# Optimization experiments

Hardware: AMD Instinct MI355X
Metric: run time of the kernel (lower is better)

## Reference

```python
import jax, jax.numpy as jnp
import numpy as np

BLANK = 0
DELAY_SCALE = 1.0
TEMPERATURE = 1.0
NEG = -1e30  # finite stand-in for -inf (safe under autodiff of cumlogsumexp)


def _delay_cost_zero(B, Tm, U1, act_lens):
    # delay_values[b, t, u] = t / act_len[b], constant over u  (delay_func='zero')
    dv = jnp.arange(Tm, dtype=jnp.float32)[None, :] / act_lens.astype(jnp.float32)[:, None]
    return jnp.broadcast_to(dv[:, :, None], (B, Tm, U1))


def _rnnt_delay_loss(acts, labels, act_lens, label_lens):
    # RNN-T forward-backward DP over the (T,U) lattice + expected-delay cost,
    # matching warp_rnnt.gpu_rnnt_delay. acts: (B,T,U+1,V) logits.
    B, Tm, U1, V = acts.shape
    U = U1 - 1
    lp = jax.nn.log_softmax(acts / TEMPERATURE, axis=-1)
    blank_lp = lp[..., BLANK]                                   # (B,Tm,U1)
    lab = jnp.broadcast_to(labels.astype(jnp.int32)[:, None, :, None], (B, Tm, U, 1))
    label_lp = jnp.take_along_axis(lp[:, :, :U, :], lab, axis=3)[..., 0]  # (B,Tm,U)
    # exclusive cumsum of label log-probs along u: Lc[...,u] = sum_{j<u} label_lp[...,j]
    Lc = jnp.concatenate([jnp.zeros((B, Tm, 1), lp.dtype), jnp.cumsum(label_lp, axis=2)], axis=2)

    # ---- alpha: alpha[t,u] = LSE(alpha[t-1,u]+blank[t-1,u], alpha[t,u-1]+label[t,u-1])
    # within-row recursion solved in closed form: alpha[t] = Lc[t] + cumlogsumexp(x - Lc[t])
    # where x[u] = alpha[t-1,u] + blank[t-1,u].
    x0 = jnp.where(jnp.arange(U1)[None, :] == 0, 0.0, NEG).astype(lp.dtype)
    alpha0 = Lc[:, 0] + jax.lax.cumlogsumexp(jnp.broadcast_to(x0, (B, U1)) - Lc[:, 0], axis=1)

    def fstep(a_prev, xs):
        bl, lc = xs
        a = lc + jax.lax.cumlogsumexp(a_prev + bl - lc, axis=1)
        return a, a

    xs = (jnp.swapaxes(blank_lp[:, :-1], 0, 1), jnp.swapaxes(Lc[:, 1:], 0, 1))
    _, alphas = jax.lax.scan(fstep, alpha0, xs)
    alpha = jnp.concatenate([alpha0[None], alphas], axis=0).swapaxes(0, 1)  # (B,Tm,U1)

    bi = jnp.arange(B)
    t_last = act_lens - 1
    logZ = alpha[bi, t_last, label_lens] + blank_lp[bi, t_last, label_lens]  # (B,)

    # ---- beta: beta[t,u] = LSE(blank[t,u]+beta[t+1,u], label[t,u]+beta[t,u+1], exit[t,u])
    # exit only at the per-example corner (act_len-1, label_len) with final blank.
    t_idx = jnp.arange(Tm)[None, :, None]
    u_idx = jnp.arange(U1)[None, None, :]
    exit_lp = jnp.where((t_idx == t_last[:, None, None]) & (u_idx == label_lens[:, None, None]), blank_lp, NEG)

    def bstep(b_next, xs):
        bl, ex, lc = xs
        y = jnp.logaddexp(bl + b_next, ex)
        b = -lc + jax.lax.cumlogsumexp(y + lc, axis=1, reverse=True)
        return b, b

    xsb = (jnp.swapaxes(blank_lp, 0, 1), jnp.swapaxes(exit_lp, 0, 1), jnp.swapaxes(Lc, 0, 1))
    _, betas = jax.lax.scan(bstep, jnp.full((B, U1), NEG, lp.dtype), xsb, reverse=True)
    beta = betas.swapaxes(0, 1)  # (B,Tm,U1)

    # ---- expected delay: posterior of emit transition (t,u)->(t,u+1)
    delay_values = _delay_cost_zero(B, Tm, U1, act_lens)
    gamma = jnp.exp(alpha[:, :, :U] + label_lp + beta[:, :, 1:] - logZ[:, None, None])  # (B,Tm,U)
    loss_delay = jnp.sum(gamma * delay_values[:, :, :U], axis=(1, 2))
    loss_rnnt = -logZ
    loss_total = loss_rnnt + DELAY_SCALE * loss_delay
    # reduction='sum'
    return loss_total.sum(), loss_rnnt.sum(), loss_delay.sum()


def setup_inputs() -> dict:
    key = jax.random.key(0)
    k1, k2, k3, k4 = jax.random.split(key, 4)
    B, Tm, U, V = 16, 256, 64, 512
    acts = jax.random.normal(k1, (B, Tm, U + 1, V), dtype=jnp.float32)
    labels = jax.random.randint(k2, (B, U), 1, V, dtype=jnp.int32)  # non-blank targets
    act_lens = jax.random.randint(k3, (B,), Tm // 2, Tm + 1, dtype=jnp.int32)
    label_lens = jax.random.randint(k4, (B,), U // 2, U + 1, dtype=jnp.int32)
    return {"acts": acts, "labels": labels, "act_lens": act_lens, "label_lens": label_lens}


def reference(acts, labels, act_lens, label_lens):
    return _rnnt_delay_loss(acts, labels, act_lens, label_lens)
```

## Files before the change

kernel.cpp:

```cpp
#include <hip/hip_runtime.h>
#include <hip/hip_bf16.h>

#define BB   16
#define TM   256
#define UU   64
#define U1   65
#define VV   512
#define ND   320
#define WROW 128
#define NEGF (-1e30f)
#define LOG2E 1.4426950408889634f
#define LN2   0.6931471805599453f

#if __has_builtin(__builtin_amdgcn_exp2f)
__device__ __forceinline__ float aexp2(float x) { return __builtin_amdgcn_exp2f(x); }
#else
__device__ __forceinline__ float aexp2(float x) { return exp2f(x); }
#endif
#if __has_builtin(__builtin_amdgcn_logf)
__device__ __forceinline__ float alog2(float x) { return __builtin_amdgcn_logf(x); }
#else
__device__ __forceinline__ float alog2(float x) { return log2f(x); }
#endif

__device__ __forceinline__ float lae2(float x, float y) {
    float m = fmaxf(x, y);
    return m + alog2(1.0f + aexp2(-fabsf(x - y)));
}
__device__ __forceinline__ float readlane_f(float v, int l) {
    return __int_as_float(__builtin_amdgcn_readlane(__float_as_int(v), l));
}
__device__ __forceinline__ float shfl_up1(float v) {
    return __int_as_float(__builtin_amdgcn_update_dpp(
        __float_as_int(v), __float_as_int(v), 0x138, 0xF, 0xF, false));
}
__device__ __forceinline__ float shfl_dn1(float v) {
    return __int_as_float(__builtin_amdgcn_update_dpp(
        __float_as_int(v), __float_as_int(v), 0x130, 0xF, 0xF, false));
}
__device__ __forceinline__ void st_clamped(float* __restrict__ s, int t, int lane, float v) {
    int tc = t < -1 ? -1 : t;
    tc = tc > 256 ? 256 : tc;
    s[(tc + 1) * UU + lane] = v;
}

__global__ void k_fill(float* __restrict__ p, int n4) {
    int i = blockIdx.x * blockDim.x + threadIdx.x;
    if (i < n4) reinterpret_cast<float4*>(p)[i] = make_float4(NEGF, NEGF, NEGF, NEGF);
}

__global__ __launch_bounds__(256) void k_lse(const float* __restrict__ acts,
                                             const int* __restrict__ labels,
                                             float* __restrict__ Aarr,
                                             float* __restrict__ Barr,
                                             float* __restrict__ p6arr,
                                             float* __restrict__ bl64) {
    int wid = (blockIdx.x << 2) + (threadIdx.x >> 6);
    if (wid >= BB * TM * U1) return;
    int lane = threadIdx.x & 63;
    const float* base = acts + (size_t)wid * VV;
    float4 va = *reinterpret_cast<const float4*>(base + lane * 4);
    float4 vb = *reinterpret_cast<const float4*>(base + 256 + lane * 4);
    float m = fmaxf(fmaxf(fmaxf(va.x, va.y), fmaxf(va.z, va.w)),
                    fmaxf(fmaxf(vb.x, vb.y), fmaxf(vb.z, vb.w)));
#pragma unroll
    for (int o = 32; o; o >>= 1) m = fmaxf(m, __shfl_xor(m, o));
    float s = __expf(va.x - m) + __expf(va.y - m) + __expf(va.z - m) + __expf(va.w - m)
            + __expf(vb.x - m) + __expf(vb.y - m) + __expf(vb.z - m) + __expf(vb.w - m);
#pragma unroll
    for (int o = 32; o; o >>= 1) s += __shfl_xor(s, o);
    float lse = m + __logf(s);
    if (lane == 0) {
        int u  = wid % U1;
        int bt = wid / U1;
        int t  = bt % TM;
        int b  = bt / TM;
        float blank = (va.x - lse) * LOG2E;
        if (u < UU) {
            int r = t + u;
            int li = labels[b * UU + u];
            float lab = (base[li] - lse) * LOG2E;
            size_t row = ((size_t)b * ND + r) * WROW;
            *reinterpret_cast<float2*>(Barr + row + 2 * u) = make_float2(lab, blank);
            Aarr[row + 2 * u] = blank;
            if (u < 63) Aarr[row + 2 * u + 3] = lab;
            else        p6arr[b * ND + r]     = lab;
        } else {
            bl64[b * TM + t] = blank;
        }
    }
}

__device__ __forceinline__ void load8s(float2 (&B)[8], const float* base,
                                       int row0, int step, int lane) {
#pragma unroll
    for (int j = 0; j < 8; ++j)
        B[j] = *reinterpret_cast<const float2*>(base + (size_t)(row0 + j * step) * WROW + 2 * lane);
}

template<bool N64>
__device__ __forceinline__ void alpha_chunk(const float2 (&B)[8], int ss0,
    int lane, int ssCap64,
    const float* __restrict__ s_bl64p, const float* __restrict__ s_p6,
    float* __restrict__ s_alpha,
    float& a, float& a64, float& cap64)
{
    float c64r[8], p6r[8], aout[8];
    if (N64) {
#pragma unroll
        for (int j = 0; j < 8; ++j) {
            int i64 = ss0 + j - 64; i64 = i64 < 0 ? 0 : i64;
            c64r[j] = s_bl64p[i64];
            p6r[j]  = s_p6[ss0 + j - 1];
        }
    }
#pragma unroll
    for (int j = 0; j < 8; ++j) {
        const float left = shfl_up1(a);
        const float anew = lae2(a + B[j].x, left + B[j].y);
        if (N64) {
            const float a63u = readlane_f(a, 63);
            a64 = lae2(a64 + c64r[j], a63u + p6r[j]);
            if (ss0 + j == ssCap64) cap64 = a64;
        }
        a = anew;
        aout[j] = anew;
    }
#pragma unroll
    for (int j = 0; j < 8; ++j)
        st_clamped(s_alpha, ss0 + j - lane, lane, aout[j]);
}

template<bool N64>
__device__ __forceinline__ void beta_chunk(const float2 (&B)[8], int ss0,
    int lane, int ssExit, int ssExit64, int L,
    const float* __restrict__ s_bl64p, float* __restrict__ s_pr,
    float& bt, float& b64)
{
    float c64r[8], bout[8];
    if (N64) {
#pragma unroll
        for (int j = 0; j < 8; ++j) {
            int i64 = ss0 - j - 63; i64 = i64 < 0 ? 0 : i64;
            c64r[j] = s_bl64p[i64];
        }
    }
#pragma unroll
    for (int j = 0; j < 8; ++j) {
        const int ss = ss0 - j;
        float right = shfl_dn1(bt);
        right = (lane == 63) ? (N64 ? b64 : NEGF) : right;
        const float pr = B[j].x + right;
        float bnew = lae2(B[j].y + bt, pr);
        if (ss == ssExit) {
            if (lane == L) bnew = lae2(bnew, B[j].y);
        }
        if (N64) {
            float b64n = b64 + c64r[j];
            if (ss == ssExit64) b64n = lae2(b64n, c64r[j]);
            b64 = b64n;
        }
        bt = bnew; bout[j] = pr;
    }
#pragma unroll
    for (int j = 0; j < 8; ++j)
        st_clamped(s_pr, ss0 - j - lane, lane, bout[j]);
}

template<bool N64>
__device__ __forceinline__ float alpha_sweep(const float* __restrict__ Aarr,
    int lane, int t_last, int L,
    const float* __restrict__ s_bl64p, const float* __restrict__ s_p6,
    float* __restrict__ s_alpha)
{
    float a = (lane == 0) ? 0.0f : NEGF;
    float a64 = NEGF, cap64 = NEGF;
    const int ssCap64 = t_last + 64;
    float2 R0[8], R1[8], R2[8], R3[8], R4[8];
    load8s(R0, Aarr, 0, 1, lane);  load8s(R1, Aarr, 8, 1, lane);
    load8s(R2, Aarr, 16, 1, lane); load8s(R3, Aarr, 24, 1, lane);
    load8s(R4, Aarr, 32, 1, lane);
    for (int c = 0; c < 40; c += 5) {
        alpha_chunk<N64>(R0, c * 8 + 1, lane, ssCap64, s_bl64p, s_p6, s_alpha, a, a64, cap64);
        if (c + 5 < 40) load8s(R0, Aarr, (c + 5) * 8, 1, lane);
        alpha_chunk<N64>(R1, (c + 1) * 8 + 1, lane, ssCap64, s_bl64p, s_p6, s_alpha, a, a64, cap64);
        if (c + 6 < 40) load8s(R1, Aarr, (c + 6) * 8, 1, lane);
        alpha_chunk<N64>(R2, (c + 2) * 8 + 1, lane, ssCap64, s_bl64p, s_p6, s_alpha, a, a64, cap64);
        if (c + 7 < 40) load8s(R2, Aarr, (c + 7) * 8, 1, lane);
        alpha_chunk<N64>(R3, (c + 3) * 8 + 1, lane, ssCap64, s_bl64p, s_p6, s_alpha, a, a64, cap64);
        if (c + 8 < 40) load8s(R3, Aarr, (c + 8) * 8, 1, lane);
        alpha_chunk<N64>(R4, (c + 4) * 8 + 1, lane, ssCap64, s_bl64p, s_p6, s_alpha, a, a64, cap64);
        if (c + 9 < 40) load8s(R4, Aarr, (c + 9) * 8, 1, lane);
    }
    return cap64;
}

template<bool N64>
__device__ __forceinline__ void beta_sweep(const float* __restrict__ Barr,
    int lane, int ssExit, int ssExit64, int L,
    const float* __restrict__ s_bl64p, float* __restrict__ s_pr)
{
    float bt = NEGF, b64 = NEGF;
    float2 R0[8], R1[8], R2[8], R3[8], R4[8];
    load8s(R0, Barr, 319, -1, lane); load8s(R1, Barr, 311, -1, lane);
    load8s(R2, Barr, 303, -1, lane); load8s(R3, Barr, 295, -1, lane);
    load8s(R4, Barr, 287, -1, lane);
    for (int c = 0; c < 40; c += 5) {
        beta_chunk<N64>(R0, 319 - c * 8, lane, ssExit, ssExit64, L, s_bl64p, s_pr, bt, b64);
        if (c + 5 < 40) load8s(R0, Barr, 319 - (c + 5) * 8, -1, lane);
        beta_chunk<N64>(R1, 319 - (c + 1) * 8, lane, ssExit, ssExit64, L, s_bl64p, s_pr, bt, b64);
        if (c + 6 < 40) load8s(R1, Barr, 319 - (c + 6) * 8, -1, lane);
        beta_chunk<N64>(R2, 319 - (c + 2) * 8, lane, ssExit, ssExit64, L, s_bl64p, s_pr, bt, b64);
        if (c + 7 < 40) load8s(R2, Barr, 319 - (c + 7) * 8, -1, lane);
        beta_chunk<N64>(R3, 319 - (c + 3) * 8, lane, ssExit, ssExit64, L, s_bl64p, s_pr, bt, b64);
        if (c + 8 < 40) load8s(R3, Barr, 319 - (c + 8) * 8, -1, lane);
        beta_chunk<N64>(R4, 319 - (c + 4) * 8, lane, ssExit, ssExit64, L, s_bl64p, s_pr, bt, b64);
        if (c + 9 < 40) load8s(R4, Barr, 319 - (c + 9) * 8, -1, lane);
    }
}

__global__ __launch_bounds__(128, 1) void k_dp(const float* __restrict__ Aarr_,
                                               const float* __restrict__ Barr_,
                                               const float* __restrict__ p6arr_,
                                               const float* __restrict__ bl64_,
                                               const int* __restrict__ act_lens,
                                               const int* __restrict__ label_lens,
                                               float* __restrict__ partials) {
    __shared__ float s_alpha[258 * UU];
    __shared__ float s_pr[258 * UU];
    __shared__ float s_bl64p[TM + 2];
    __shared__ float s_p6[ND];
    __shared__ float s_logZ;
    __shared__ float s_red[2];
    const int b    = blockIdx.x;
    const int tid  = threadIdx.x;
    const int lane = tid & 63;
    const int wv   = tid >> 6;
    const float* Aarr = Aarr_ + (size_t)b * ND * WROW;
    const float* Barr = Barr_ + (size_t)b * ND * WROW;

    if (tid == 0) { s_bl64p[0] = NEGF; s_bl64p[TM + 1] = NEGF; }
    for (int i = tid; i < TM; i += 128) s_bl64p[i + 1] = bl64_[b * TM + i];
    for (int i = tid; i < ND; i += 128) s_p6[i] = p6arr_[b * ND + i];
    __syncthreads();

    const int T = act_lens[b];
    const int L = label_lens[b];
    const int t_last = T - 1;

    if (wv == 0) {
        if (lane == 0) s_alpha[1 * UU + 0] = 0.0f;
        float aE;
        if (L == UU) {
            aE = alpha_sweep<true >(Aarr, lane, t_last, L, s_bl64p, s_p6, s_alpha);
        } else {
            alpha_sweep<false>(Aarr, lane, t_last, L, s_bl64p, s_p6, s_alpha);
            aE = s_alpha[(t_last + 1) * UU + L];
        }
        const float blankLast = (L < UU) ? Aarr[(size_t)(t_last + L) * WROW + 2 * L]
                                         : s_bl64p[t_last + 1];
        if (lane == 0) s_logZ = aE + blankLast;
    } else {
        const int ssExit   = t_last + L;
        const int ssExit64 = (L == UU) ? (t_last + 64) : -1;
        if (L == UU) beta_sweep<true >(Barr, lane, ssExit, ssExit64, L, s_bl64p, s_pr);
        else         beta_sweep<false>(Barr, lane, ssExit, ssExit64, L, s_bl64p, s_pr);
    }
    __syncthreads();

    const float logZ = s_logZ;
    const float invT = 1.0f / (float)T;
    float dsum = 0.0f;
#pragma unroll 8
    for (int idx = tid; idx < TM * UU; idx += 128) {
        const int t = idx >> 6;
        dsum = __fmaf_rn(aexp2(s_alpha[idx + UU] + s_pr[idx + UU] - logZ),
                         (float)t * invT, dsum);
    }
#pragma unroll
    for (int o = 32; o; o >>= 1) dsum += __shfl_xor(dsum, o);
    if (lane == 0) s_red[wv] = dsum;
    __syncthreads();
    if (tid == 0) {
        partials[2 * b + 0] = -logZ * LN2;
        partials[2 * b + 1] = s_red[0] + s_red[1];
    }
}

__global__ void k_reduce(const float* __restrict__ partials, float* __restrict__ out) {
    if (threadIdx.x == 0 && blockIdx.x == 0) {
        float rn = 0.0f, dl = 0.0f;
        for (int b = 0; b < BB; ++b) {
            rn += partials[2 * b + 0];
            dl += partials[2 * b + 1];
        }
        out[0] = rn + dl;
        out[1] = rn;
        out[2] = dl;
    }
}

extern "C" void kernel_launch(void* const* d_in, const int* in_sizes, int n_in,
                              void* d_out, int out_size, void* d_ws, size_t ws_size,
                              hipStream_t stream) {
    const float* acts       = (const float*)d_in[0];
    const int*   labels     = (const int*)d_in[1];
    const int*   act_lens   = (const int*)d_in[2];
    const int*   label_lens = (const int*)d_in[3];

    float* ws       = (float*)d_ws;
    float* Aarr     = ws;
    float* Barr     = Aarr + (size_t)BB * ND * WROW;
    float* p6arr    = Barr + (size_t)BB * ND * WROW;
    float* bl64     = p6arr + BB * ND;
    float* partials = bl64 + BB * TM;

    const int nfill4 = (2 * BB * ND * WROW + BB * ND) / 4;
    k_fill<<<(nfill4 + 255) / 256, 256, 0, stream>>>(ws, nfill4);

    const int rows = BB * TM * U1;
    k_lse<<<(rows + 3) / 4, 256, 0, stream>>>(acts, labels, Aarr, Barr, p6arr, bl64);
    k_dp<<<BB, 128, 0, stream>>>(Aarr, Barr, p6arr, bl64, act_lens, label_lens, partials);
    k_reduce<<<1, 64, 0, stream>>>(partials, (float*)d_out);
}
```

Measured before the change: 140.8 us.

## Run RNN-T DP in scaled probability space instead of log space

The alpha/beta recursions now work on probabilities with per-wave exponent rescaling every four steps, instead of log-add-exp. Each step becomes an FMA plus a DPP shuffle rather than an exp and a log, and k_lse stores probabilities instead of log-probs. The separate column-64 tracking is replaced by a precomputed cumulative log-blank boundary for beta, and logZ is read from beta at the origin. This adds scale bookkeeping (a DPP max-reduction and a readlane) on the serial chain, and it risks precision loss or underflow compared with log-space arithmetic.

```diff
diff --git a/kernel.cpp b/kernel.cpp
--- a/kernel.cpp
+++ b/kernel.cpp
@@ -9,8 +9,7 @@
 #define ND   320
 #define WROW 128
 #define NEGF (-1e30f)
-#define LOG2E 1.4426950408889634f
-#define LN2   0.6931471805599453f
+#define LN2  0.6931471805599453f
 
 #if __has_builtin(__builtin_amdgcn_exp2f)
 __device__ __forceinline__ float aexp2(float x) { return __builtin_amdgcn_exp2f(x); }
@@ -22,11 +21,8 @@
 #else
 __device__ __forceinline__ float alog2(float x) { return log2f(x); }
 #endif
-
-__device__ __forceinline__ float lae2(float x, float y) {
-    float m = fmaxf(x, y);
-    return m + alog2(1.0f + aexp2(-fabsf(x - y)));
-}
+__device__ __forceinline__ float alog2c(float x) { return fmaxf(alog2(x), NEGF); }
+
 __device__ __forceinline__ float readlane_f(float v, int l) {
     return __int_as_float(__builtin_amdgcn_readlane(__float_as_int(v), l));
 }
@@ -37,6 +33,29 @@
 __device__ __forceinline__ float shfl_dn1(float v) {
     return __int_as_float(__builtin_amdgcn_update_dpp(
         __float_as_int(v), __float_as_int(v), 0x130, 0xF, 0xF, false));
+}
+template<int CTRL>
+__device__ __forceinline__ float dppmax(float v) {
+    int x = __builtin_amdgcn_update_dpp(__float_as_int(v), __float_as_int(v),
+                                        CTRL, 0xF, 0xF, false);
+    return fmaxf(v, __int_as_float(x));
+}
+__device__ __forceinline__ void applyscale(float& v, int& E, float cmx) {
+    float m = cmx;
+    m = dppmax<0x111>(m);
+    m = dppmax<0x112>(m);
+    m = dppmax<0x114>(m);
+    m = dppmax<0x118>(m);
+    m = dppmax<0x142>(m);
+    m = dppmax<0x143>(m);
+    int smx = __builtin_amdgcn_readlane(__float_as_int(m), 63);
+    if (smx != 0) {
+        int e = ((smx >> 23) & 0xFF) - 127;
+        if (e < -27) e = -27;
+        float sc = __int_as_float((227 - e) << 23);
+        v *= sc;
+        E += e - 100;
+    }
 }
 __device__ __forceinline__ void st_clamped(float* __restrict__ s, int t, int lane, float v) {
     int tc = t < -1 ? -1 : t;
@@ -44,16 +63,10 @@
     s[(tc + 1) * UU + lane] = v;
 }
 
-__global__ void k_fill(float* __restrict__ p, int n4) {
-    int i = blockIdx.x * blockDim.x + threadIdx.x;
-    if (i < n4) reinterpret_cast<float4*>(p)[i] = make_float4(NEGF, NEGF, NEGF, NEGF);
-}
-
 __global__ __launch_bounds__(256) void k_lse(const float* __restrict__ acts,
                                              const int* __restrict__ labels,
                                              float* __restrict__ Aarr,
                                              float* __restrict__ Barr,
-                                             float* __restrict__ p6arr,
                                              float* __restrict__ bl64) {
     int wid = (blockIdx.x << 2) + (threadIdx.x >> 6);
     if (wid >= BB * TM * U1) return;
@@ -69,24 +82,23 @@
             + __expf(vb.x - m) + __expf(vb.y - m) + __expf(vb.z - m) + __expf(vb.w - m);
 #pragma unroll
     for (int o = 32; o; o >>= 1) s += __shfl_xor(s, o);
-    float lse = m + __logf(s);
+    float rcp_s = 1.0f / s;
     if (lane == 0) {
         int u  = wid % U1;
         int bt = wid / U1;
         int t  = bt % TM;
         int b  = bt / TM;
-        float blank = (va.x - lse) * LOG2E;
+        float pblank = __expf(va.x - m) * rcp_s;
         if (u < UU) {
             int r = t + u;
             int li = labels[b * UU + u];
-            float lab = (base[li] - lse) * LOG2E;
+            float plab = __expf(base[li] - m) * rcp_s;
             size_t row = ((size_t)b * ND + r) * WROW;
-            *reinterpret_cast<float2*>(Barr + row + 2 * u) = make_float2(lab, blank);
-            Aarr[row + 2 * u] = blank;
-            if (u < 63) Aarr[row + 2 * u + 3] = lab;
-            else        p6arr[b * ND + r]     = lab;
+            *reinterpret_cast<float2*>(Barr + row + 2 * u) = make_float2(plab, pblank);
+            Aarr[row + 2 * u] = pblank;
+            if (u < 63) Aarr[row + 2 * u + 3] = plab;
         } else {
-            bl64[b * TM + t] = blank;
+            bl64[b * TM + t] = pblank;
         }
     }
 }
@@ -98,138 +110,94 @@
         B[j] = *reinterpret_cast<const float2*>(base + (size_t)(row0 + j * step) * WROW + 2 * lane);
 }
 
-template<bool N64>
-__device__ __forceinline__ void alpha_chunk(const float2 (&B)[8], int ss0,
-    int lane, int ssCap64,
-    const float* __restrict__ s_bl64p, const float* __restrict__ s_p6,
-    float* __restrict__ s_alpha,
-    float& a, float& a64, float& cap64)
+__device__ __forceinline__ void alpha_chunk(const float2 (&B)[8], int ss0, int ck,
+    int lane, float* __restrict__ s_alpha, float* __restrict__ s_Ea,
+    float& a, int& E)
 {
-    float c64r[8], p6r[8], aout[8];
-    if (N64) {
-#pragma unroll
-        for (int j = 0; j < 8; ++j) {
-            int i64 = ss0 + j - 64; i64 = i64 < 0 ? 0 : i64;
-            c64r[j] = s_bl64p[i64];
-            p6r[j]  = s_p6[ss0 + j - 1];
-        }
-    }
-#pragma unroll
-    for (int j = 0; j < 8; ++j) {
+    float aout[8];
+    float cmx = a;
+    if (lane == 0) s_Ea[2 * ck] = (float)E;
+#pragma unroll
+    for (int j = 0; j < 4; ++j) {
         const float left = shfl_up1(a);
-        const float anew = lae2(a + B[j].x, left + B[j].y);
-        if (N64) {
-            const float a63u = readlane_f(a, 63);
-            a64 = lae2(a64 + c64r[j], a63u + p6r[j]);
-            if (ss0 + j == ssCap64) cap64 = a64;
-        }
-        a = anew;
-        aout[j] = anew;
-    }
+        a = __fmaf_rn(a, B[j].x, left * B[j].y);
+        aout[j] = a;
+    }
+    applyscale(a, E, cmx);
+    cmx = a;
+    if (lane == 0) s_Ea[2 * ck + 1] = (float)E;
+#pragma unroll
+    for (int j = 4; j < 8; ++j) {
+        const float left = shfl_up1(a);
+        a = __fmaf_rn(a, B[j].x, left * B[j].y);
+        aout[j] = a;
+    }
+    applyscale(a, E, cmx);
 #pragma unroll
     for (int j = 0; j < 8; ++j)
         st_clamped(s_alpha, ss0 + j - lane, lane, aout[j]);
 }
 
 template<bool N64>
-__device__ __forceinline__ void beta_chunk(const float2 (&B)[8], int ss0,
-    int lane, int ssExit, int ssExit64, int L,
-    const float* __restrict__ s_bl64p, float* __restrict__ s_pr,
-    float& bt, float& b64)
+__device__ __forceinline__ void beta_chunk(const float2 (&B)[8], int ss0, int ck,
+    int lane, int ssExit, int L,
+    float* __restrict__ s_pr, float* __restrict__ s_Eb,
+    const float* __restrict__ s_b64, float& b, int& E)
 {
-    float c64r[8], bout[8];
+    float prout[8];
+    float cmx = b;
+    if (lane == 0) s_Eb[2 * ck] = (float)E;
+    float r64[8];
     if (N64) {
 #pragma unroll
-        for (int j = 0; j < 8; ++j) {
-            int i64 = ss0 - j - 63; i64 = i64 < 0 ? 0 : i64;
-            c64r[j] = s_bl64p[i64];
-        }
-    }
-#pragma unroll
-    for (int j = 0; j < 8; ++j) {
+        for (int j = 0; j < 4; ++j)
+            r64[j] = aexp2(fminf(s_b64[ss0 - j + 1] - (float)E, 126.0f));
+    }
+#pragma unroll
+    for (int j = 0; j < 4; ++j) {
         const int ss = ss0 - j;
-        float right = shfl_dn1(bt);
-        right = (lane == 63) ? (N64 ? b64 : NEGF) : right;
-        const float pr = B[j].x + right;
-        float bnew = lae2(B[j].y + bt, pr);
-        if (ss == ssExit) {
-            if (lane == L) bnew = lae2(bnew, B[j].y);
-        }
-        if (N64) {
-            float b64n = b64 + c64r[j];
-            if (ss == ssExit64) b64n = lae2(b64n, c64r[j]);
-            b64 = b64n;
-        }
-        bt = bnew; bout[j] = pr;
-    }
+        float right = shfl_dn1(b);
+        right = (lane == 63) ? (N64 ? r64[j] : 0.0f) : right;
+        const float pr = B[j].x * right;
+        b = __fmaf_rn(b, B[j].y, pr);
+        if (ss == ssExit) { if (lane == L) b += B[j].y; }
+        prout[j] = pr;
+    }
+    applyscale(b, E, cmx);
+    cmx = b;
+    if (lane == 0) s_Eb[2 * ck + 1] = (float)E;
+    if (N64) {
+#pragma unroll
+        for (int j = 4; j < 8; ++j)
+            r64[j] = aexp2(fminf(s_b64[ss0 - j + 1] - (float)E, 126.0f));
+    }
+#pragma unroll
+    for (int j = 4; j < 8; ++j) {
+        const int ss = ss0 - j;
+        float right = shfl_dn1(b);
+        right = (lane == 63) ? (N64 ? r64[j] : 0.0f) : right;
+        const float pr = B[j].x * right;
+        b = __fmaf_rn(b, B[j].y, pr);
+        if (ss == ssExit) { if (lane == L) b += B[j].y; }
+        prout[j] = pr;
+    }
+    applyscale(b, E, cmx);
 #pragma unroll
     for (int j = 0; j < 8; ++j)
-        st_clamped(s_pr, ss0 - j - lane, lane, bout[j]);
-}
-
-template<bool N64>
-__device__ __forceinline__ float alpha_sweep(const float* __restrict__ Aarr,
-    int lane, int t_last, int L,
-    const float* __restrict__ s_bl64p, const float* __restrict__ s_p6,
-    float* __restrict__ s_alpha)
-{
-    float a = (lane == 0) ? 0.0f : NEGF;
-    float a64 = NEGF, cap64 = NEGF;
-    const int ssCap64 = t_last + 64;
-    float2 R0[8], R1[8], R2[8], R3[8], R4[8];
-    load8s(R0, Aarr, 0, 1, lane);  load8s(R1, Aarr, 8, 1, lane);
-    load8s(R2, Aarr, 16, 1, lane); load8s(R3, Aarr, 24, 1, lane);
-    load8s(R4, Aarr, 32, 1, lane);
-    for (int c = 0; c < 40; c += 5) {
-        alpha_chunk<N64>(R0, c * 8 + 1, lane, ssCap64, s_bl64p, s_p6, s_alpha, a, a64, cap64);
-        if (c + 5 < 40) load8s(R0, Aarr, (c + 5) * 8, 1, lane);
-        alpha_chunk<N64>(R1, (c + 1) * 8 + 1, lane, ssCap64, s_bl64p, s_p6, s_alpha, a, a64, cap64);
-        if (c + 6 < 40) load8s(R1, Aarr, (c + 6) * 8, 1, lane);
-        alpha_chunk<N64>(R2, (c + 2) * 8 + 1, lane, ssCap64, s_bl64p, s_p6, s_alpha, a, a64, cap64);
-        if (c + 7 < 40) load8s(R2, Aarr, (c + 7) * 8, 1, lane);
-        alpha_chunk<N64>(R3, (c + 3) * 8 + 1, lane, ssCap64, s_bl64p, s_p6, s_alpha, a, a64, cap64);
-        if (c + 8 < 40) load8s(R3, Aarr, (c + 8) * 8, 1, lane);
-        alpha_chunk<N64>(R4, (c + 4) * 8 + 1, lane, ssCap64, s_bl64p, s_p6, s_alpha, a, a64, cap64);
-        if (c + 9 < 40) load8s(R4, Aarr, (c + 9) * 8, 1, lane);
-    }
-    return cap64;
-}
-
-template<bool N64>
-__device__ __forceinline__ void beta_sweep(const float* __restrict__ Barr,
-    int lane, int ssExit, int ssExit64, int L,
-    const float* __restrict__ s_bl64p, float* __restrict__ s_pr)
-{
-    float bt = NEGF, b64 = NEGF;
-    float2 R0[8], R1[8], R2[8], R3[8], R4[8];
-    load8s(R0, Barr, 319, -1, lane); load8s(R1, Barr, 311, -1, lane);
-    load8s(R2, Barr, 303, -1, lane); load8s(R3, Barr, 295, -1, lane);
-    load8s(R4, Barr, 287, -1, lane);
-    for (int c = 0; c < 40; c += 5) {
-        beta_chunk<N64>(R0, 319 - c * 8, lane, ssExit, ssExit64, L, s_bl64p, s_pr, bt, b64);
-        if (c + 5 < 40) load8s(R0, Barr, 319 - (c + 5) * 8, -1, lane);
-        beta_chunk<N64>(R1, 319 - (c + 1) * 8, lane, ssExit, ssExit64, L, s_bl64p, s_pr, bt, b64);
-        if (c + 6 < 40) load8s(R1, Barr, 319 - (c + 6) * 8, -1, lane);
-        beta_chunk<N64>(R2, 319 - (c + 2) * 8, lane, ssExit, ssExit64, L, s_bl64p, s_pr, bt, b64);
-        if (c + 7 < 40) load8s(R2, Barr, 319 - (c + 7) * 8, -1, lane);
-        beta_chunk<N64>(R3, 319 - (c + 3) * 8, lane, ssExit, ssExit64, L, s_bl64p, s_pr, bt, b64);
-        if (c + 8 < 40) load8s(R3, Barr, 319 - (c + 8) * 8, -1, lane);
-        beta_chunk<N64>(R4, 319 - (c + 4) * 8, lane, ssExit, ssExit64, L, s_bl64p, s_pr, bt, b64);
-        if (c + 9 < 40) load8s(R4, Barr, 319 - (c + 9) * 8, -1, lane);
-    }
+        st_clamped(s_pr, ss0 - j - lane, lane, prout[j]);
 }
 
 __global__ __launch_bounds__(128, 1) void k_dp(const float* __restrict__ Aarr_,
                                                const float* __restrict__ Barr_,
-                                               const float* __restrict__ p6arr_,
                                                const float* __restrict__ bl64_,
                                                const int* __restrict__ act_lens,
                                                const int* __restrict__ label_lens,
                                                float* __restrict__ partials) {
     __shared__ float s_alpha[258 * UU];
     __shared__ float s_pr[258 * UU];
-    __shared__ float s_bl64p[TM + 2];
-    __shared__ float s_p6[ND];
+    __shared__ float s_bl64[TM];
+    __shared__ float s_b64[ND + 1];
+    __shared__ float s_Ea[80], s_Eb[80];
     __shared__ float s_logZ;
     __shared__ float s_red[2];
     const int b    = blockIdx.x;
@@ -239,9 +207,7 @@
     const float* Aarr = Aarr_ + (size_t)b * ND * WROW;
     const float* Barr = Barr_ + (size_t)b * ND * WROW;
 
-    if (tid == 0) { s_bl64p[0] = NEGF; s_bl64p[TM + 1] = NEGF; }
-    for (int i = tid; i < TM; i += 128) s_bl64p[i + 1] = bl64_[b * TM + i];
-    for (int i = tid; i < ND; i += 128) s_p6[i] = p6arr_[b * ND + i];
+    for (int i = tid; i < TM; i += 128) s_bl64[i] = bl64_[b * TM + i];
     __syncthreads();
 
     const int T = act_lens[b];
@@ -249,40 +215,93 @@
     const int t_last = T - 1;
 
     if (wv == 0) {
-        if (lane == 0) s_alpha[1 * UU + 0] = 0.0f;
-        float aE;
+        float a = (lane == 0) ? 1.0f : 0.0f;
+        int E = 0;
+        st_clamped(s_alpha, 0 - lane, lane, a);
+        float2 R0[8], R1[8], R2[8], R3[8], R4[8];
+        load8s(R0, Aarr, 0, 1, lane);  load8s(R1, Aarr, 8, 1, lane);
+        load8s(R2, Aarr, 16, 1, lane); load8s(R3, Aarr, 24, 1, lane);
+        load8s(R4, Aarr, 32, 1, lane);
+        for (int c = 0; c < 40; c += 5) {
+            alpha_chunk(R0, c * 8 + 1, c, lane, s_alpha, s_Ea, a, E);
+            if (c + 5 < 40) load8s(R0, Aarr, (c + 5) * 8, 1, lane);
+            alpha_chunk(R1, (c + 1) * 8 + 1, c + 1, lane, s_alpha, s_Ea, a, E);
+            if (c + 6 < 40) load8s(R1, Aarr, (c + 6) * 8, 1, lane);
+            alpha_chunk(R2, (c + 2) * 8 + 1, c + 2, lane, s_alpha, s_Ea, a, E);
+            if (c + 7 < 40) load8s(R2, Aarr, (c + 7) * 8, 1, lane);
+            alpha_chunk(R3, (c + 3) * 8 + 1, c + 3, lane, s_alpha, s_Ea, a, E);
+            if (c + 8 < 40) load8s(R3, Aarr, (c + 8) * 8, 1, lane);
+            alpha_chunk(R4, (c + 4) * 8 + 1, c + 4, lane, s_alpha, s_Ea, a, E);
+            if (c + 9 < 40) load8s(R4, Aarr, (c + 9) * 8, 1, lane);
+        }
+    } else {
+        for (int i = lane; i <= ND; i += 64) s_b64[i] = NEGF;
+        if (L == UU && lane == 0) {
+            float run = 0.0f;
+            for (int t = t_last; t >= 0; --t) {
+                run += alog2c(s_bl64[t]);
+                s_b64[t + 64] = run;
+            }
+        }
+        float bt = 0.0f;
+        int Eb = 0;
+        const int ssExit = (L < UU) ? (t_last + L) : -1;
+        float2 R0[8], R1[8], R2[8], R3[8], R4[8];
+        load8s(R0, Barr, 319, -1, lane); load8s(R1, Barr, 311, -1, lane);
+        load8s(R2, Barr, 303, -1, lane); load8s(R3, Barr, 295, -1, lane);
+        load8s(R4, Barr, 287, -1, lane);
         if (L == UU) {
-            aE = alpha_sweep<true >(Aarr, lane, t_last, L, s_bl64p, s_p6, s_alpha);
+            for (int c = 0; c < 40; c += 5) {
+                beta_chunk<true>(R0, 319 - c * 8, c, lane, ssExit, L, s_pr, s_Eb, s_b64, bt, Eb);
+                if (c + 5 < 40) load8s(R0, Barr, 319 - (c + 5) * 8, -1, lane);
+                beta_chunk<true>(R1, 319 - (c + 1) * 8, c + 1, lane, ssExit, L, s_pr, s_Eb, s_b64, bt, Eb);
+                if (c + 6 < 40) load8s(R1, Barr, 319 - (c + 6) * 8, -1, lane);
+                beta_chunk<true>(R2, 319 - (c + 2) * 8, c + 2, lane, ssExit, L, s_pr, s_Eb, s_b64, bt, Eb);
+                if (c + 7 < 40) load8s(R2, Barr, 319 - (c + 7) * 8, -1, lane);
+                beta_chunk<true>(R3, 319 - (c + 3) * 8, c + 3, lane, ssExit, L, s_pr, s_Eb, s_b64, bt, Eb);
+                if (c + 8 < 40) load8s(R3, Barr, 319 - (c + 8) * 8, -1, lane);
+                beta_chunk<true>(R4, 319 - (c + 4) * 8, c + 4, lane, ssExit, L, s_pr, s_Eb, s_b64, bt, Eb);
+                if (c + 9 < 40) load8s(R4, Barr, 319 - (c + 9) * 8, -1, lane);
+            }
         } else {
-            alpha_sweep<false>(Aarr, lane, t_last, L, s_bl64p, s_p6, s_alpha);
-            aE = s_alpha[(t_last + 1) * UU + L];
-        }
-        const float blankLast = (L < UU) ? Aarr[(size_t)(t_last + L) * WROW + 2 * L]
-                                         : s_bl64p[t_last + 1];
-        if (lane == 0) s_logZ = aE + blankLast;
-    } else {
-        const int ssExit   = t_last + L;
-        const int ssExit64 = (L == UU) ? (t_last + 64) : -1;
-        if (L == UU) beta_sweep<true >(Barr, lane, ssExit, ssExit64, L, s_bl64p, s_pr);
-        else         beta_sweep<false>(Barr, lane, ssExit, ssExit64, L, s_bl64p, s_pr);
+            for (int c = 0; c < 40; c += 5) {
+                beta_chunk<false>(R0, 319 - c * 8, c, lane, ssExit, L, s_pr, s_Eb, s_b64, bt, Eb);
+                if (c + 5 < 40) load8s(R0, Barr, 319 - (c + 5) * 8, -1, lane);
+                beta_chunk<false>(R1, 319 - (c + 1) * 8, c + 1, lane, ssExit, L, s_pr, s_Eb, s_b64, bt, Eb);
+                if (c + 6 < 40) load8s(R1, Barr, 319 - (c + 6) * 8, -1, lane);
+                beta_chunk<false>(R2, 319 - (c + 2) * 8, c + 2, lane, ssExit, L, s_pr, s_Eb, s_b64, bt, Eb);
+                if (c + 7 < 40) load8s(R2, Barr, 319 - (c + 7) * 8, -1, lane);
+                beta_chunk<false>(R3, 319 - (c + 3) * 8, c + 3, lane, ssExit, L, s_pr, s_Eb, s_b64, bt, Eb);
+                if (c + 8 < 40) load8s(R3, Barr, 319 - (c + 8) * 8, -1, lane);
+                beta_chunk<false>(R4, 319 - (c + 4) * 8, c + 4, lane, ssExit, L, s_pr, s_Eb, s_b64, bt, Eb);
+                if (c + 9 < 40) load8s(R4, Barr, 319 - (c + 9) * 8, -1, lane);
+            }
+        }
+        const float b0 = readlane_f(bt, 0);
+        if (lane == 0) s_logZ = alog2c(b0) + (float)Eb;
     }
     __syncthreads();
 
-    const float logZ = s_logZ;
+    const float logZ2 = s_logZ;
     const float invT = 1.0f / (float)T;
     float dsum = 0.0f;
-#pragma unroll 8
+#pragma unroll 4
     for (int idx = tid; idx < TM * UU; idx += 128) {
-        const int t = idx >> 6;
-        dsum = __fmaf_rn(aexp2(s_alpha[idx + UU] + s_pr[idx + UU] - logZ),
-                         (float)t * invT, dsum);
+        const int t = idx >> 6, u = idx & 63, d = t + u;
+        const int ca = (d > 0 ? d - 1 : 0) >> 2;
+        const int cb = (319 - d) >> 2;
+        const float a2 = alog2c(s_alpha[idx + UU]) + s_Ea[ca];
+        const float p2 = alog2c(s_pr[idx + UU]) + s_Eb[cb];
+        float g = a2 + p2 - logZ2;
+        g = fminf(g, 0.0f);
+        dsum = __fmaf_rn(aexp2(g), (float)t * invT, dsum);
     }
 #pragma unroll
     for (int o = 32; o; o >>= 1) dsum += __shfl_xor(dsum, o);
     if (lane == 0) s_red[wv] = dsum;
     __syncthreads();
     if (tid == 0) {
-        partials[2 * b + 0] = -logZ * LN2;
+        partials[2 * b + 0] = -logZ2 * LN2;
         partials[2 * b + 1] = s_red[0] + s_red[1];
     }
 }
@@ -311,15 +330,14 @@
     float* ws       = (float*)d_ws;
     float* Aarr     = ws;
     float* Barr     = Aarr + (size_t)BB * ND * WROW;
-    float* p6arr    = Barr + (size_t)BB * ND * WROW;
-    float* bl64     = p6arr + BB * ND;
+    float* bl64     = Barr + (size_t)BB * ND * WROW;
     float* partials = bl64 + BB * TM;
 
-    const int nfill4 = (2 * BB * ND * WROW + BB * ND) / 4;
-    k_fill<<<(nfill4 + 255) / 256, 256, 0, stream>>>(ws, nfill4);
+    size_t zbytes = (size_t)(2 * BB * ND * WROW) * sizeof(float);
+    (void)hipMemsetAsync(ws, 0, zbytes, stream);
 
     const int rows = BB * TM * U1;
-    k_lse<<<(rows + 3) / 4, 256, 0, stream>>>(acts, labels, Aarr, Barr, p6arr, bl64);
-    k_dp<<<BB, 128, 0, stream>>>(Aarr, Barr, p6arr, bl64, act_lens, label_lens, partials);
+    k_lse<<<(rows + 3) / 4, 256, 0, stream>>>(acts, labels, Aarr, Barr, bl64);
+    k_dp<<<BB, 128, 0, stream>>>(Aarr, Barr, bl64, act_lens, label_lens, partials);
     k_reduce<<<1, 64, 0, stream>>>(partials, (float*)d_out);
 }
```

New measurement: 145.6 us. 1.03x slower.
